# Kernel tuning notes

Hardware: AMD Instinct MI355X
Metric: run time of the kernel (lower is better)

## Reference

```python
import jax, jax.numpy as jnp
import numpy as np

IN_DIM = 64  # channels; theta/phi -> C//8, g -> C//2


def _maxpool2x2(t):
    # t: [B, c, H, W] -> [B, c, H//2, W//2]
    B, c, H, W = t.shape
    return t.reshape(B, c, H // 2, 2, W // 2, 2).max(axis=(3, 5))


def setup_inputs() -> dict:
    key = jax.random.key(0)
    ks = jax.random.split(key, 6)
    C = IN_DIM
    x = jax.random.normal(ks[0], (16, C, 64, 64), dtype=jnp.float32)
    # 1x1 convs stored as [out, in] matrices (kernel is 1x1, no bias)
    w_theta = jax.random.normal(ks[1], (C // 8, C), dtype=jnp.float32) * (1.0 / np.sqrt(C))
    w_phi = jax.random.normal(ks[2], (C // 8, C), dtype=jnp.float32) * (1.0 / np.sqrt(C))
    w_g = jax.random.normal(ks[3], (C // 2, C), dtype=jnp.float32) * (1.0 / np.sqrt(C))
    w_o = jax.random.normal(ks[4], (C, C // 2), dtype=jnp.float32) * (1.0 / np.sqrt(C // 2))
    gamma = jax.random.normal(ks[5], (), dtype=jnp.float32)  # torch inits to 0; nonzero for testing
    return {"x": x, "w_theta": w_theta, "w_phi": w_phi, "w_g": w_g, "w_o": w_o, "gamma": gamma}


def reference(x, w_theta, w_phi, w_g, w_o, gamma):
    B, C, H, W = x.shape
    # 1x1 conv projections (pointwise channel matmuls)
    theta = jnp.einsum('oc,bchw->bohw', w_theta, x).reshape(B, C // 8, H * W)
    phi = _maxpool2x2(jnp.einsum('oc,bchw->bohw', w_phi, x)).reshape(B, C // 8, H * W // 4)
    g = _maxpool2x2(jnp.einsum('oc,bchw->bohw', w_g, x)).reshape(B, C // 2, H * W // 4)
    # attention: [B, HW, HW/4]
    beta = jax.nn.softmax(jnp.einsum('bcn,bcm->bnm', theta, phi), axis=-1)
    # aggregate values: g @ beta^T -> [B, C//2, HW]
    o = jnp.einsum('bcm,bnm->bcn', g, beta).reshape(B, C // 2, H, W)
    o = jnp.einsum('oc,bchw->bohw', w_o, o)
    return gamma * o + x
```

## Files before the change

### kernel.cpp

```cpp
#include <hip/hip_runtime.h>

typedef _Float16 half4v __attribute__((ext_vector_type(4)));
typedef _Float16 h2     __attribute__((ext_vector_type(2)));
typedef float    float4v __attribute__((ext_vector_type(4)));

#define BB 16
#define CC 64
#define NN 4096
#define MM 1024
#define LN256 5.545177444479562f

static __device__ __forceinline__ float4v mfma16(half4v a, half4v b, float4v c) {
    return __builtin_amdgcn_mfma_f32_16x16x16f16(a, b, c, 0, 0, 0);
}

__device__ __forceinline__ unsigned pk2(float a, float b) {
    union { _Float16 h[2]; unsigned u; } cv;
    cv.h[0] = (_Float16)a; cv.h[1] = (_Float16)b;
    return cv.u;
}
__device__ __forceinline__ h2 ash2(unsigned u) {
    union { unsigned u; h2 h; } c; c.u = u; return c.h;
}
__device__ __forceinline__ h2 hmax2(h2 a, h2 b) {
    h2 r;
    r.x = (a.x > b.x) ? a.x : b.x;
    r.y = (a.y > b.y) ? a.y : b.y;
    return r;
}
__device__ __forceinline__ h2 shfl_xor_h2(h2 v, int m) {
    union { h2 h; int i; } c; c.h = v; c.i = __shfl_xor(c.i, m);
    return c.h;
}

__global__ __launch_bounds__(128, 4) void proj_kernel(
    const float* __restrict__ x,
    const float* __restrict__ w_th,
    const float* __restrict__ w_ph,
    const float* __restrict__ w_g,
    _Float16* __restrict__ theta,
    _Float16* __restrict__ phi,
    _Float16* __restrict__ gT)
{
    __shared__ __align__(16) float wlds[64 * 16];
    unsigned* wl2 = (unsigned*)wlds;

    const int b   = blockIdx.y;
    const int blk = blockIdx.x;
    const int z   = blockIdx.z;
    const int t   = threadIdx.x;

    if (z == 0) {
        for (int i = t; i < 1024; i += 128) {
            int c = i >> 4, o = i & 15;
            wlds[i] = (o < 8) ? w_th[o * 64 + c] : w_ph[(o - 8) * 64 + c];
        }
    } else {
        for (int i = t; i < 1024; i += 128) {
            int c = i >> 4, o2 = i & 15;
            wl2[i] = pk2(w_g[(2 * o2) * 64 + c], w_g[(2 * o2 + 1) * 64 + c]);
        }
    }
    __syncthreads();

    const float2* x2 = (const float2*)(x + (size_t)b * CC * NN);
    const int p2 = blk * 128 + t;
    const int l = t & 63, w = t >> 6;
    const int m = (blk * 2 + w) * 32 + (l & 31);

    if (z == 0) {
        float th0[8], th1[8], ph0[8], ph1[8];
#pragma unroll
        for (int i = 0; i < 8; i++) { th0[i]=th1[i]=ph0[i]=ph1[i]=0.f; }
#pragma unroll 4
        for (int c = 0; c < 64; c++) {
            float2 xv = x2[c * (NN / 2) + p2];
            const float4* w4 = (const float4*)&wlds[c * 16];
            float4 wv[4];
#pragma unroll
            for (int j = 0; j < 4; j++) wv[j] = w4[j];
            const float* wf = (const float*)wv;
#pragma unroll
            for (int o = 0; o < 8; o++) {
                th0[o] = fmaf(wf[o], xv.x, th0[o]);
                th1[o] = fmaf(wf[o], xv.y, th1[o]);
                ph0[o] = fmaf(wf[8 + o], xv.x, ph0[o]);
                ph1[o] = fmaf(wf[8 + o], xv.y, ph1[o]);
            }
        }
        uint4* tw = (uint4*)(theta + ((size_t)b * NN + 2 * p2) * 8);
        tw[0] = make_uint4(pk2(th0[0],th0[1]), pk2(th0[2],th0[3]),
                           pk2(th0[4],th0[5]), pk2(th0[6],th0[7]));
        tw[1] = make_uint4(pk2(th1[0],th1[1]), pk2(th1[2],th1[3]),
                           pk2(th1[4],th1[5]), pk2(th1[6],th1[7]));
        float phm[8];
#pragma unroll
        for (int i = 0; i < 8; i++) phm[i] = fmaxf(ph0[i], ph1[i]);
#pragma unroll
        for (int i = 0; i < 8; i++) phm[i] = fmaxf(phm[i], __shfl_xor(phm[i], 32));
        if (l < 32) {
            uint4* pw = (uint4*)(phi + ((size_t)b * MM + m) * 8);
            pw[0] = make_uint4(pk2(phm[0],phm[1]), pk2(phm[2],phm[3]),
                               pk2(phm[4],phm[5]), pk2(phm[6],phm[7]));
        }
    } else {
        h2 ga[16], gb[16];
#pragma unroll
        for (int i = 0; i < 16; i++) { ga[i] = (h2)0; gb[i] = (h2)0; }
#pragma unroll 4
        for (int c = 0; c < 64; c++) {
            float2 xv = x2[c * (NN / 2) + p2];
            const uint4* w4 = (const uint4*)&wl2[c * 16];
            uint4 q0 = w4[0], q1 = w4[1], q2 = w4[2], q3 = w4[3];
            unsigned wv[16] = {q0.x,q0.y,q0.z,q0.w, q1.x,q1.y,q1.z,q1.w,
                               q2.x,q2.y,q2.z,q2.w, q3.x,q3.y,q3.z,q3.w};
            _Float16 hx = (_Float16)xv.x, hy = (_Float16)xv.y;
            h2 xa; xa.x = hx; xa.y = hx;
            h2 xb; xb.x = hy; xb.y = hy;
#pragma unroll
            for (int k = 0; k < 16; k++) {
                ga[k] = __builtin_elementwise_fma(ash2(wv[k]), xa, ga[k]);
                gb[k] = __builtin_elementwise_fma(ash2(wv[k]), xb, gb[k]);
            }
        }
        h2 gm[16];
#pragma unroll
        for (int k = 0; k < 16; k++) gm[k] = hmax2(ga[k], gb[k]);
#pragma unroll
        for (int k = 0; k < 16; k++) gm[k] = hmax2(gm[k], shfl_xor_h2(gm[k], 32));
        const int k0 = (l < 32) ? 0 : 8;
        _Float16* gp = gT + ((size_t)b * 32 + 2 * k0) * MM + m;
#pragma unroll
        for (int k = 0; k < 8; k++) {
            h2 v = gm[k0 + k];
            gp[(size_t)(2 * k) * MM]     = v.x;
            gp[(size_t)(2 * k + 1) * MM] = v.y;
        }
    }
}

__global__ __launch_bounds__(256, 4) void attn_kernel(
    const _Float16* __restrict__ theta,
    const _Float16* __restrict__ phi,
    const _Float16* __restrict__ gT,
    const float* __restrict__ w_o,
    const float* __restrict__ gamma_p,
    const float* __restrict__ x,
    float* __restrict__ out)
{
    __shared__ __align__(16) _Float16 phl[MM * 8];
    __shared__ __align__(16) _Float16 gl[32 * 136];

    const int b    = blockIdx.y;
    const int t    = threadIdx.x;
    const int wave = t >> 6;
    const int lane = t & 63;
    const int col  = lane & 15;
    const int q    = lane >> 4;
    const int nbase = blockIdx.x * 64 + wave * 16;

    const float4v zero4 = {0.f, 0.f, 0.f, 0.f};
    const half4v zeroh = {0, 0, 0, 0};

    {
        const float4* src = (const float4*)(phi + (size_t)b * MM * 8);
        float4* dst = (float4*)phl;
#pragma unroll
        for (int i = 0; i < 4; i++) dst[t + i * 256] = src[t + i * 256];
    }

    half4v thB = zeroh;
    if (q < 2)
        thB = *(const half4v*)(theta + ((size_t)b * NN + nbase + col) * 8 + q * 4);

    half4v onesA = zeroh;
    if (col == 0) {
        onesA[0] = (_Float16)1; onesA[1] = (_Float16)1;
        onesA[2] = (_Float16)1; onesA[3] = (_Float16)1;
    }

    __syncthreads();

    float mx = -1e30f;
#pragma unroll 4
    for (int mt = 0; mt < 64; mt++) {
        half4v af = zeroh;
        if (q < 2)
            af = *(const half4v*)&phl[(mt * 16 + col) * 8 + q * 4];
        float4v S = mfma16(af, thB, zero4);
        mx = fmaxf(mx, fmaxf(fmaxf(S.x, S.y), fmaxf(S.z, S.w)));
    }
    mx = fmaxf(mx, __shfl_xor(mx, 16));
    mx = fmaxf(mx, __shfl_xor(mx, 32));
    const float shift = mx - LN256;

    float4v acc0 = zero4, acc1 = zero4, accd = zero4;

    for (int m0 = 0; m0 < MM; m0 += 128) {
        __syncthreads();
        {
            int c = t >> 3, seg = (t & 7) * 16;
            const _Float16* src = gT + ((size_t)b * 32 + c) * MM + m0 + seg;
            float4 v0 = *(const float4*)src;
            float4 v1 = *(const float4*)(src + 8);
            *(float4*)&gl[c * 136 + seg]     = v0;
            *(float4*)&gl[c * 136 + seg + 8] = v1;
        }
        __syncthreads();

#pragma unroll 2
        for (int mt = 0; mt < 8; mt++) {
            half4v af = zeroh;
            if (q < 2)
                af = *(const half4v*)&phl[(m0 + mt * 16 + col) * 8 + q * 4];
            float4v S = mfma16(af, thB, zero4);
            half4v P;
            P[0] = (_Float16)__expf(S.x - shift);
            P[1] = (_Float16)__expf(S.y - shift);
            P[2] = (_Float16)__expf(S.z - shift);
            P[3] = (_Float16)__expf(S.w - shift);
            half4v ag0 = *(const half4v*)&gl[col * 136 + mt * 16 + q * 4];
            half4v ag1 = *(const half4v*)&gl[(col + 16) * 136 + mt * 16 + q * 4];
            acc0 = mfma16(ag0, P, acc0);
            acc1 = mfma16(ag1, P, acc1);
            accd = mfma16(onesA, P, accd);
        }
    }

    float dv = __shfl(accd.x, col);
    float sc = gamma_p[0] / dv;

    half4v B0, B1;
    B0[0] = (_Float16)(acc0.x * sc); B0[1] = (_Float16)(acc0.y * sc);
    B0[2] = (_Float16)(acc0.z * sc); B0[3] = (_Float16)(acc0.w * sc);
    B1[0] = (_Float16)(acc1.x * sc); B1[1] = (_Float16)(acc1.y * sc);
    B1[2] = (_Float16)(acc1.z * sc); B1[3] = (_Float16)(acc1.w * sc);

#pragma unroll
    for (int ct = 0; ct < 4; ct++) {
        const float* wp = w_o + (size_t)(ct * 16 + col) * 32 + q * 4;
        float4 w0 = *(const float4*)wp;
        float4 w1 = *(const float4*)(wp + 16);
        half4v wa, wb;
        wa[0] = (_Float16)w0.x; wa[1] = (_Float16)w0.y;
        wa[2] = (_Float16)w0.z; wa[3] = (_Float16)w0.w;
        wb[0] = (_Float16)w1.x; wb[1] = (_Float16)w1.y;
        wb[2] = (_Float16)w1.z; wb[3] = (_Float16)w1.w;
        float4v D = mfma16(wa, B0, zero4);
        D = mfma16(wb, B1, D);
#pragma unroll
        for (int r = 0; r < 4; r++) {
            int co = ct * 16 + q * 4 + r;
            size_t idx = ((size_t)b * CC + co) * NN + nbase + col;
            out[idx] = D[r] + x[idx];
        }
    }
}

extern "C" void kernel_launch(void* const* d_in, const int* in_sizes, int n_in,
                              void* d_out, int out_size, void* d_ws, size_t ws_size,
                              hipStream_t stream) {
    const float* x       = (const float*)d_in[0];
    const float* w_theta = (const float*)d_in[1];
    const float* w_phi   = (const float*)d_in[2];
    const float* w_g     = (const float*)d_in[3];
    const float* w_o     = (const float*)d_in[4];
    const float* gamma   = (const float*)d_in[5];
    float* out = (float*)d_out;

    _Float16* theta_ws = (_Float16*)d_ws;
    _Float16* phi_ws   = theta_ws + (size_t)BB * NN * 8;
    _Float16* gT_ws    = phi_ws   + (size_t)BB * MM * 8;

    proj_kernel<<<dim3(16, BB, 2), 128, 0, stream>>>(
        x, w_theta, w_phi, w_g, theta_ws, phi_ws, gT_ws);

    attn_kernel<<<dim3(NN / 64, BB), 256, 0, stream>>>(
        theta_ws, phi_ws, gT_ws, w_o, gamma, x, out);
}
```

Before: 118.7 us.

## Process two query tiles per wave and double-buffer the g tile in LDS

Each wave now handles 32 query columns instead of 16. Every phi fragment and every g fragment loaded from LDS is therefore reused for two score tiles, and the phi staging per block is amortised over twice as many queries. The g tile staging becomes double-buffered, with one barrier per chunk instead of two, so the next chunk's global load can overlap compute. The cost is higher register pressure (launch bounds lowered to 2 blocks/CU), more LDS, and half as many blocks (512) on the device.

```diff
diff --git a/kernel.cpp b/kernel.cpp
--- a/kernel.cpp
+++ b/kernel.cpp
@@ -139,7 +139,7 @@
     }
 }
 
-__global__ __launch_bounds__(256, 4) void attn_kernel(
+__global__ __launch_bounds__(256, 2) void attn_kernel(
     const _Float16* __restrict__ theta,
     const _Float16* __restrict__ phi,
     const _Float16* __restrict__ gT,
@@ -149,7 +149,7 @@
     float* __restrict__ out)
 {
     __shared__ __align__(16) _Float16 phl[MM * 8];
-    __shared__ __align__(16) _Float16 gl[32 * 136];
+    __shared__ __align__(16) _Float16 gl[2][32 * 136];
 
     const int b    = blockIdx.y;
     const int t    = threadIdx.x;
@@ -157,7 +157,7 @@
     const int lane = t & 63;
     const int col  = lane & 15;
     const int q    = lane >> 4;
-    const int nbase = blockIdx.x * 64 + wave * 16;
+    const int nbase = blockIdx.x * 128 + wave * 32;
 
     const float4v zero4 = {0.f, 0.f, 0.f, 0.f};
     const half4v zeroh = {0, 0, 0, 0};
@@ -169,9 +169,11 @@
         for (int i = 0; i < 4; i++) dst[t + i * 256] = src[t + i * 256];
     }
 
-    half4v thB = zeroh;
-    if (q < 2)
-        thB = *(const half4v*)(theta + ((size_t)b * NN + nbase + col) * 8 + q * 4);
+    half4v thB0 = zeroh, thB1 = zeroh;
+    if (q < 2) {
+        thB0 = *(const half4v*)(theta + ((size_t)b * NN + nbase + col) * 8 + q * 4);
+        thB1 = *(const half4v*)(theta + ((size_t)b * NN + nbase + 16 + col) * 8 + q * 4);
+    }
 
     half4v onesA = zeroh;
     if (col == 0) {
@@ -181,60 +183,85 @@
 
     __syncthreads();
 
-    float mx = -1e30f;
+    float mx0 = -1e30f, mx1 = -1e30f;
 #pragma unroll 4
     for (int mt = 0; mt < 64; mt++) {
         half4v af = zeroh;
         if (q < 2)
             af = *(const half4v*)&phl[(mt * 16 + col) * 8 + q * 4];
-        float4v S = mfma16(af, thB, zero4);
-        mx = fmaxf(mx, fmaxf(fmaxf(S.x, S.y), fmaxf(S.z, S.w)));
-    }
-    mx = fmaxf(mx, __shfl_xor(mx, 16));
-    mx = fmaxf(mx, __shfl_xor(mx, 32));
-    const float shift = mx - LN256;
-
-    float4v acc0 = zero4, acc1 = zero4, accd = zero4;
-
-    for (int m0 = 0; m0 < MM; m0 += 128) {
-        __syncthreads();
-        {
-            int c = t >> 3, seg = (t & 7) * 16;
-            const _Float16* src = gT + ((size_t)b * 32 + c) * MM + m0 + seg;
-            float4 v0 = *(const float4*)src;
-            float4 v1 = *(const float4*)(src + 8);
-            *(float4*)&gl[c * 136 + seg]     = v0;
-            *(float4*)&gl[c * 136 + seg + 8] = v1;
-        }
-        __syncthreads();
+        float4v S0 = mfma16(af, thB0, zero4);
+        float4v S1 = mfma16(af, thB1, zero4);
+        mx0 = fmaxf(mx0, fmaxf(fmaxf(S0.x, S0.y), fmaxf(S0.z, S0.w)));
+        mx1 = fmaxf(mx1, fmaxf(fmaxf(S1.x, S1.y), fmaxf(S1.z, S1.w)));
+    }
+    mx0 = fmaxf(mx0, __shfl_xor(mx0, 16));
+    mx0 = fmaxf(mx0, __shfl_xor(mx0, 32));
+    mx1 = fmaxf(mx1, __shfl_xor(mx1, 16));
+    mx1 = fmaxf(mx1, __shfl_xor(mx1, 32));
+    const float shift0 = mx0 - LN256;
+    const float shift1 = mx1 - LN256;
+
+    float4v a00 = zero4, a01 = zero4, accd0 = zero4;
+    float4v a10 = zero4, a11 = zero4, accd1 = zero4;
+
+    const int sc_c = t >> 3, sc_s = (t & 7) * 16;
+    {
+        const _Float16* src = gT + ((size_t)b * 32 + sc_c) * MM + sc_s;
+        *(float4*)&gl[0][sc_c * 136 + sc_s]     = *(const float4*)src;
+        *(float4*)&gl[0][sc_c * 136 + sc_s + 8] = *(const float4*)(src + 8);
+    }
+    __syncthreads();
+
+    for (int c8 = 0; c8 < 8; c8++) {
+        const int cur = c8 & 1;
+        if (c8 < 7) {
+            const _Float16* src =
+                gT + ((size_t)b * 32 + sc_c) * MM + (c8 + 1) * 128 + sc_s;
+            *(float4*)&gl[1 - cur][sc_c * 136 + sc_s]     = *(const float4*)src;
+            *(float4*)&gl[1 - cur][sc_c * 136 + sc_s + 8] = *(const float4*)(src + 8);
+        }
 
 #pragma unroll 2
         for (int mt = 0; mt < 8; mt++) {
             half4v af = zeroh;
             if (q < 2)
-                af = *(const half4v*)&phl[(m0 + mt * 16 + col) * 8 + q * 4];
-            float4v S = mfma16(af, thB, zero4);
-            half4v P;
-            P[0] = (_Float16)__expf(S.x - shift);
-            P[1] = (_Float16)__expf(S.y - shift);
-            P[2] = (_Float16)__expf(S.z - shift);
-            P[3] = (_Float16)__expf(S.w - shift);
-            half4v ag0 = *(const half4v*)&gl[col * 136 + mt * 16 + q * 4];
-            half4v ag1 = *(const half4v*)&gl[(col + 16) * 136 + mt * 16 + q * 4];
-            acc0 = mfma16(ag0, P, acc0);
-            acc1 = mfma16(ag1, P, acc1);
-            accd = mfma16(onesA, P, accd);
-        }
-    }
-
-    float dv = __shfl(accd.x, col);
-    float sc = gamma_p[0] / dv;
-
-    half4v B0, B1;
-    B0[0] = (_Float16)(acc0.x * sc); B0[1] = (_Float16)(acc0.y * sc);
-    B0[2] = (_Float16)(acc0.z * sc); B0[3] = (_Float16)(acc0.w * sc);
-    B1[0] = (_Float16)(acc1.x * sc); B1[1] = (_Float16)(acc1.y * sc);
-    B1[2] = (_Float16)(acc1.z * sc); B1[3] = (_Float16)(acc1.w * sc);
+                af = *(const half4v*)&phl[(c8 * 128 + mt * 16 + col) * 8 + q * 4];
+            float4v S0 = mfma16(af, thB0, zero4);
+            float4v S1 = mfma16(af, thB1, zero4);
+            half4v P0, P1;
+            P0[0] = (_Float16)__expf(S0.x - shift0);
+            P0[1] = (_Float16)__expf(S0.y - shift0);
+            P0[2] = (_Float16)__expf(S0.z - shift0);
+            P0[3] = (_Float16)__expf(S0.w - shift0);
+            P1[0] = (_Float16)__expf(S1.x - shift1);
+            P1[1] = (_Float16)__expf(S1.y - shift1);
+            P1[2] = (_Float16)__expf(S1.z - shift1);
+            P1[3] = (_Float16)__expf(S1.w - shift1);
+            half4v ag0 = *(const half4v*)&gl[cur][col * 136 + mt * 16 + q * 4];
+            half4v ag1 = *(const half4v*)&gl[cur][(col + 16) * 136 + mt * 16 + q * 4];
+            a00 = mfma16(ag0, P0, a00);
+            a01 = mfma16(ag1, P0, a01);
+            a10 = mfma16(ag0, P1, a10);
+            a11 = mfma16(ag1, P1, a11);
+            accd0 = mfma16(onesA, P0, accd0);
+            accd1 = mfma16(onesA, P1, accd1);
+        }
+        __syncthreads();
+    }
+
+    const float gamma = gamma_p[0];
+    float sc0 = gamma / __shfl(accd0.x, col);
+    float sc1 = gamma / __shfl(accd1.x, col);
+
+    half4v B00, B01, B10, B11;
+    B00[0] = (_Float16)(a00.x * sc0); B00[1] = (_Float16)(a00.y * sc0);
+    B00[2] = (_Float16)(a00.z * sc0); B00[3] = (_Float16)(a00.w * sc0);
+    B01[0] = (_Float16)(a01.x * sc0); B01[1] = (_Float16)(a01.y * sc0);
+    B01[2] = (_Float16)(a01.z * sc0); B01[3] = (_Float16)(a01.w * sc0);
+    B10[0] = (_Float16)(a10.x * sc1); B10[1] = (_Float16)(a10.y * sc1);
+    B10[2] = (_Float16)(a10.z * sc1); B10[3] = (_Float16)(a10.w * sc1);
+    B11[0] = (_Float16)(a11.x * sc1); B11[1] = (_Float16)(a11.y * sc1);
+    B11[2] = (_Float16)(a11.z * sc1); B11[3] = (_Float16)(a11.w * sc1);
 
 #pragma unroll
     for (int ct = 0; ct < 4; ct++) {
@@ -246,13 +273,16 @@
         wa[2] = (_Float16)w0.z; wa[3] = (_Float16)w0.w;
         wb[0] = (_Float16)w1.x; wb[1] = (_Float16)w1.y;
         wb[2] = (_Float16)w1.z; wb[3] = (_Float16)w1.w;
-        float4v D = mfma16(wa, B0, zero4);
-        D = mfma16(wb, B1, D);
+        float4v D0 = mfma16(wa, B00, zero4);
+        D0 = mfma16(wb, B01, D0);
+        float4v D1 = mfma16(wa, B10, zero4);
+        D1 = mfma16(wb, B11, D1);
 #pragma unroll
         for (int r = 0; r < 4; r++) {
             int co = ct * 16 + q * 4 + r;
-            size_t idx = ((size_t)b * CC + co) * NN + nbase + col;
-            out[idx] = D[r] + x[idx];
+            size_t i0 = ((size_t)b * CC + co) * NN + nbase + col;
+            out[i0] = D0[r] + x[i0];
+            out[i0 + 16] = D1[r] + x[i0 + 16];
         }
     }
 }
@@ -275,6 +305,6 @@
     proj_kernel<<<dim3(16, BB, 2), 128, 0, stream>>>(
         x, w_theta, w_phi, w_g, theta_ws, phi_ws, gT_ws);
 
-    attn_kernel<<<dim3(NN / 64, BB), 256, 0, stream>>>(
+    attn_kernel<<<dim3(NN / 128, BB), 256, 0, stream>>>(
         theta_ws, phi_ws, gT_ws, w_o, gamma, x, out);
 }
```

Measured after the change: 120.4 us. Within noise of the previous version (+1.5%).
